# Kernel tuning notes

Measured on AMD Instinct MI355X. Metric: run time of the kernel, lower is better.

The kernel has to match this reference:

```python
import jax, jax.numpy as jnp
import numpy as np

N_NODES = 200000
N_EDGES = 3200000
DIM = 64


def setup_inputs() -> dict:
    key = jax.random.key(0)
    ks = jax.random.split(key, 8)
    ego = jax.random.normal(ks[0], (N_NODES, DIM), dtype=jnp.float32) * 0.1
    W1 = jax.random.normal(ks[1], (DIM, DIM), dtype=jnp.float32) * (1.0 / np.sqrt(DIM))
    b1 = jnp.zeros((DIM,), dtype=jnp.float32)
    W2 = jax.random.normal(ks[2], (DIM, DIM), dtype=jnp.float32) * (1.0 / np.sqrt(DIM))
    b2 = jnp.zeros((DIM,), dtype=jnp.float32)
    edge_row = jax.random.randint(ks[3], (N_EDGES,), 0, N_NODES, dtype=jnp.int32)
    edge_col = jax.random.randint(ks[4], (N_EDGES,), 0, N_NODES, dtype=jnp.int32)
    edge_val = jax.random.uniform(ks[5], (N_EDGES,), dtype=jnp.float32)
    return {"ego_embeddings": ego, "W1": W1, "b1": b1, "W2": W2, "b2": b2,
            "edge_row": edge_row, "edge_col": edge_col, "edge_val": edge_val}


def reference(ego_embeddings, W1, b1, W2, b2, edge_row, edge_col, edge_val):
    # side = A_in @ ego : sparse COO matmul via gather + weighted segment-sum
    gathered = ego_embeddings[edge_col] * edge_val[:, None]        # [E, D]
    side = jax.ops.segment_sum(gathered, edge_row, num_segments=N_NODES)  # [N, D]
    # bi-interaction aggregator (KGAT): LeakyReLU(negative_slope=0.01)
    sum_emb = jax.nn.leaky_relu((ego_embeddings + side) @ W1 + b1)
    bi_emb = jax.nn.leaky_relu((ego_embeddings * side) @ W2 + b2)
    return sum_emb + bi_emb  # dropout=0.0 -> identity
```

## Files before the change

kernel.cpp:

```cpp
#include <hip/hip_runtime.h>

#define DIM 64
#define SCAN_T 256
#define SCAN_E 8
#define SCAN_CHUNK (SCAN_T * SCAN_E)
#define BSHIFT 9
#define BROWS (1 << BSHIFT)
#define PBLK 512
#define MAXBUK 512

typedef unsigned int u32;
typedef unsigned long long u64;
typedef unsigned short u16;

__device__ __forceinline__ u32 packCV(int col, float v) {
    int q = (int)(v * 16384.f + 0.5f);
    q = min(q, 16383);
    return ((u32)col << 14) | (u32)q;
}

__device__ __forceinline__ u16 f2bf(float f) {
    u32 u = __float_as_uint(f);
    u32 r = u + 0x7FFFu + ((u >> 16) & 1u);
    return (u16)(r >> 16);
}
__device__ __forceinline__ float bf2f(u16 h) {
    return __uint_as_float((u32)h << 16);
}

__global__ void cvt_k(const float* __restrict__ src, u16* __restrict__ dst, int n4) {
    int i = blockIdx.x * blockDim.x + threadIdx.x;
    if (i < n4) {
        float4 f = reinterpret_cast<const float4*>(src)[i];
        ushort4 h;
        h.x = f2bf(f.x); h.y = f2bf(f.y); h.z = f2bf(f.z); h.w = f2bf(f.w);
        reinterpret_cast<ushort4*>(dst)[i] = h;
    }
}


__global__ __launch_bounds__(256) void histb_k(const int* __restrict__ erow,
                                               int* __restrict__ bhist,
                                               int E, int CH, int nbuk) {
    __shared__ int h[MAXBUK];
    const int tid = threadIdx.x;
    for (int i = tid; i < nbuk; i += 256) h[i] = 0;
    __syncthreads();
    const int s = blockIdx.x * CH;
    const int e = min(E, s + CH);
    for (int i4 = s + tid * 4; i4 < e; i4 += 256 * 4) {
        if (i4 + 3 < e) {
            const int4 r = *reinterpret_cast<const int4*>(erow + i4);
            atomicAdd(&h[r.x >> BSHIFT], 1);
            atomicAdd(&h[r.y >> BSHIFT], 1);
            atomicAdd(&h[r.z >> BSHIFT], 1);
            atomicAdd(&h[r.w >> BSHIFT], 1);
        } else {
            for (int i = i4; i < e; ++i) atomicAdd(&h[erow[i] >> BSHIFT], 1);
        }
    }
    __syncthreads();
    for (int i = tid; i < nbuk; i += 256) bhist[i * PBLK + blockIdx.x] = h[i];
}

__global__ void bbase_k(int* __restrict__ bhist, int* __restrict__ bktTot) {
    __shared__ int sh[SCAN_T];
    const int bk  = blockIdx.x;
    const int tid = threadIdx.x;
    const int v0 = bhist[bk * PBLK + 2 * tid];
    const int v1 = bhist[bk * PBLK + 2 * tid + 1];
    sh[tid] = v0 + v1;
    __syncthreads();
    for (int off = 1; off < SCAN_T; off <<= 1) {
        int t = (tid >= off) ? sh[tid - off] : 0;
        __syncthreads();
        sh[tid] += t;
        __syncthreads();
    }
    const int excl = (tid == 0) ? 0 : sh[tid - 1];
    bhist[bk * PBLK + 2 * tid]     = excl;
    bhist[bk * PBLK + 2 * tid + 1] = excl + v0;
    if (tid == SCAN_T - 1) bktTot[bk] = sh[SCAN_T - 1];
}

__global__ void scanBk_k(const int* __restrict__ tot, int* __restrict__ base, int nbuk) {
    __shared__ int sh[MAXBUK + 1];
    const int tid = threadIdx.x;
    for (int i = tid; i < nbuk; i += 512) sh[i] = tot[i];
    __syncthreads();
    if (tid == 0) {
        int s = 0;
        for (int i = 0; i < nbuk; ++i) { int t = sh[i]; sh[i] = s; s += t; }
        sh[nbuk] = s;
    }
    __syncthreads();
    for (int i = tid; i <= nbuk; i += 512) base[i] = sh[i];
}

__global__ __launch_bounds__(256) void part_k(const int* __restrict__ erow,
                                              const int* __restrict__ ecol,
                                              const float* __restrict__ ev,
                                              const int* __restrict__ bhist,
                                              const int* __restrict__ bktBase,
                                              u32* __restrict__ tcv,
                                              u16* __restrict__ trow,
                                              int E, int CH, int nbuk) {
    __shared__ int cur[MAXBUK];
    const int tid = threadIdx.x;
    for (int i = tid; i < nbuk; i += 256)
        cur[i] = bktBase[i] + bhist[i * PBLK + blockIdx.x];
    __syncthreads();
    const int s = blockIdx.x * CH;
    const int e = min(E, s + CH);
    const int lm = BROWS - 1;
    for (int i4 = s + tid * 4; i4 < e; i4 += 256 * 4) {
        if (i4 + 3 < e) {
            const int4   r = *reinterpret_cast<const int4*>(erow + i4);
            const int4   c = *reinterpret_cast<const int4*>(ecol + i4);
            const float4 v = *reinterpret_cast<const float4*>(ev + i4);
            int p;
            p = atomicAdd(&cur[r.x >> BSHIFT], 1); tcv[p] = packCV(c.x, v.x); trow[p] = (u16)(r.x & lm);
            p = atomicAdd(&cur[r.y >> BSHIFT], 1); tcv[p] = packCV(c.y, v.y); trow[p] = (u16)(r.y & lm);
            p = atomicAdd(&cur[r.z >> BSHIFT], 1); tcv[p] = packCV(c.z, v.z); trow[p] = (u16)(r.z & lm);
            p = atomicAdd(&cur[r.w >> BSHIFT], 1); tcv[p] = packCV(c.w, v.w); trow[p] = (u16)(r.w & lm);
        } else {
            for (int i = i4; i < e; ++i) {
                const int r = erow[i];
                const int p = atomicAdd(&cur[r >> BSHIFT], 1);
                tcv[p] = packCV(ecol[i], ev[i]);
                trow[p] = (u16)(r & lm);
            }
        }
    }
}

__global__ __launch_bounds__(512) void final2_k(const u32* __restrict__ tcv,
                                                const u16* __restrict__ trow,
                                                const int* __restrict__ bktBase,
                                                int* __restrict__ offs,
                                                u32* __restrict__ scv,
                                                int N, int nbuk) {
    __shared__ int rcur[BROWS];
    __shared__ int sc[BROWS];
    const int tid  = threadIdx.x;
    const int bk   = blockIdx.x;
    const int row0 = bk << BSHIFT;
    const int rows = min(BROWS, N - row0);
    const int s = bktBase[bk];
    const int e = bktBase[bk + 1];
    rcur[tid] = 0;
    __syncthreads();
    for (int i = s + tid; i < e; i += 512) atomicAdd(&rcur[trow[i]], 1);
    __syncthreads();
    sc[tid] = rcur[tid];
    __syncthreads();
    for (int off = 1; off < BROWS; off <<= 1) {
        int t = (tid >= off) ? sc[tid - off] : 0;
        __syncthreads();
        sc[tid] += t;
        __syncthreads();
    }
    const int excl = (tid == 0) ? 0 : sc[tid - 1];
    rcur[tid] = s + excl;
    if (tid < rows) offs[row0 + tid] = s + excl;
    if (bk == nbuk - 1 && tid == 0) offs[N] = e;
    __syncthreads();
    for (int i = s + tid; i < e; i += 512) {
        const u32 cv = tcv[i];
        const int lr = trow[i];
        const int p = atomicAdd(&rcur[lr], 1);
        scv[p] = cv;
    }
}

__global__ void hist_k(const int* __restrict__ erow, int* __restrict__ cnt, int E) {
    const int e4 = (blockIdx.x * blockDim.x + threadIdx.x) * 4;
    if (e4 + 3 < E) {
        const int4 r = *reinterpret_cast<const int4*>(erow + e4);
        atomicAdd(&cnt[r.x], 1);
        atomicAdd(&cnt[r.y], 1);
        atomicAdd(&cnt[r.z], 1);
        atomicAdd(&cnt[r.w], 1);
    } else {
        for (int e = e4; e < E; ++e) atomicAdd(&cnt[erow[e]], 1);
    }
}

__global__ void scanA_k(const int* __restrict__ cnt, int* __restrict__ offs,
                        int* __restrict__ bsums, int N) {
    __shared__ int sh[SCAN_T];
    const int base = blockIdx.x * SCAN_CHUNK + threadIdx.x * SCAN_E;
    int v[SCAN_E];
    int s = 0;
#pragma unroll
    for (int j = 0; j < SCAN_E; ++j) {
        int idx = base + j;
        int c = (idx < N) ? cnt[idx] : 0;
        v[j] = s;
        s += c;
    }
    sh[threadIdx.x] = s;
    __syncthreads();
    for (int off = 1; off < SCAN_T; off <<= 1) {
        int t = (threadIdx.x >= off) ? sh[threadIdx.x - off] : 0;
        __syncthreads();
        sh[threadIdx.x] += t;
        __syncthreads();
    }
    const int excl = (threadIdx.x == 0) ? 0 : sh[threadIdx.x - 1];
    if (threadIdx.x == SCAN_T - 1) bsums[blockIdx.x] = sh[SCAN_T - 1];
#pragma unroll
    for (int j = 0; j < SCAN_E; ++j) {
        int idx = base + j;
        if (idx < N) offs[idx] = v[j] + excl;
    }
}

__global__ void scanB_k(int* __restrict__ bsums, int nb) {
    __shared__ int sh[1024];
    const int tid = threadIdx.x;
    if (tid < nb) sh[tid] = bsums[tid];
    __syncthreads();
    if (tid == 0) {
        int s = 0;
        for (int i = 0; i < nb; ++i) { int t = sh[i]; sh[i] = s; s += t; }
    }
    __syncthreads();
    if (tid < nb) bsums[tid] = sh[tid];
}

__global__ void scanC_k(int* __restrict__ offs, int* __restrict__ cursor,
                        const int* __restrict__ bsums, int N, int E) {
    const int i = blockIdx.x * blockDim.x + threadIdx.x;
    if (i < N) {
        int v = offs[i] + bsums[i / SCAN_CHUNK];
        offs[i] = v;
        cursor[i] = v;
    }
    if (i == 0) offs[N] = E;
}

__global__ void reorder_k(const int* __restrict__ erow, const int* __restrict__ ecol,
                          const float* __restrict__ ev, int* __restrict__ cursor,
                          u32* __restrict__ scv, int E) {
    const int e4 = (blockIdx.x * blockDim.x + threadIdx.x) * 4;
    if (e4 + 3 < E) {
        const int4   r = *reinterpret_cast<const int4*>(erow + e4);
        const int4   c = *reinterpret_cast<const int4*>(ecol + e4);
        const float4 v = *reinterpret_cast<const float4*>(ev + e4);
        int p;
        p = atomicAdd(&cursor[r.x], 1); scv[p] = packCV(c.x, v.x);
        p = atomicAdd(&cursor[r.y], 1); scv[p] = packCV(c.y, v.y);
        p = atomicAdd(&cursor[r.z], 1); scv[p] = packCV(c.z, v.z);
        p = atomicAdd(&cursor[r.w], 1); scv[p] = packCV(c.w, v.w);
    } else {
        for (int e = e4; e < E; ++e) {
            int p = atomicAdd(&cursor[erow[e]], 1);
            scv[p] = packCV(ecol[e], ev[e]);
        }
    }
}

__device__ __forceinline__ float lrelu(float x) {
    return fmaxf(x, 0.f) + 0.01f * fminf(x, 0.f);
}

template <bool BF16>
__global__ __launch_bounds__(256, 2) void fused_k(const float* __restrict__ ego,
                                                  const u16* __restrict__ egoh,
                                                  const float* __restrict__ W1,
                                                  const float* __restrict__ b1,
                                                  const float* __restrict__ W2,
                                                  const float* __restrict__ b2,
                                                  const int* __restrict__ offs,
                                                  const u32* __restrict__ scv,
                                                  float* __restrict__ out,
                                                  int N, int rowsPerWave) {
    __shared__ __align__(16) float xsh[4][2][DIM];
    const int lane = threadIdx.x & 63;
    const int wid  = threadIdx.x >> 6;

    float w1[DIM], w2[DIM];
#pragma unroll
    for (int k = 0; k < DIM; ++k) {
        w1[k] = W1[k * DIM + lane];
        w2[k] = W2[k * DIM + lane];
    }
    const float bb1 = b1[lane];
    const float bb2 = b2[lane];

    const int waveId = blockIdx.x * 4 + wid;
    const int r0 = waveId * rowsPerWave;
    const int r1 = min(N, r0 + rowsPerWave);

    for (int row = r0; row < r1; ++row) {
        const int s = offs[row];
        const int t = offs[row + 1];
        float acc = 0.f;
        for (int base = s; base < t; base += 64) {
            const int m = min(64, t - base);
            const u32 cv = (lane < m) ? scv[base + lane] : 0u;
            for (int j = 0; j < m; j += 8) {
                u32 uu[8];
#pragma unroll
                for (int i = 0; i < 8; ++i) {
                    const int sj = j + i;
                    const u32 x = (u32)__shfl((int)cv, sj & 63);
                    uu[i] = (sj < m) ? x : 0u;
                }
                float g[8];
#pragma unroll
                for (int i = 0; i < 8; ++i) {
                    if (BF16) g[i] = bf2f(egoh[(uu[i] >> 14) * DIM + lane]);
                    else      g[i] = ego[(uu[i] >> 14) * DIM + lane];
                }
                const float sc = 1.f / 16384.f;
#pragma unroll
                for (int i = 0; i < 8; ++i)
                    acc = fmaf((float)(uu[i] & 16383u) * sc, g[i], acc);
            }
        }
        const int obase = row * DIM + lane;
        const float e = ego[obase];
        xsh[wid][0][lane] = e + acc;
        xsh[wid][1][lane] = e * acc;
        float a1 = bb1, a2 = bb2;
#pragma unroll
        for (int k4 = 0; k4 < 16; ++k4) {
            const float4 xa = *reinterpret_cast<const float4*>(&xsh[wid][0][k4 * 4]);
            const float4 xm = *reinterpret_cast<const float4*>(&xsh[wid][1][k4 * 4]);
            a1 = fmaf(xa.x, w1[4 * k4 + 0], a1);
            a1 = fmaf(xa.y, w1[4 * k4 + 1], a1);
            a1 = fmaf(xa.z, w1[4 * k4 + 2], a1);
            a1 = fmaf(xa.w, w1[4 * k4 + 3], a1);
            a2 = fmaf(xm.x, w2[4 * k4 + 0], a2);
            a2 = fmaf(xm.y, w2[4 * k4 + 1], a2);
            a2 = fmaf(xm.z, w2[4 * k4 + 2], a2);
            a2 = fmaf(xm.w, w2[4 * k4 + 3], a2);
        }
        out[obase] = lrelu(a1) + lrelu(a2);
    }
}

__device__ __forceinline__ void atomAddF(float* p, float v) {
    __hip_atomic_fetch_add(p, v, __ATOMIC_RELAXED, __HIP_MEMORY_SCOPE_AGENT);
}

__global__ void scatter_k(const float* __restrict__ ego,
                          const int* __restrict__ erow,
                          const int* __restrict__ ecol,
                          const float* __restrict__ eval_,
                          float* __restrict__ side,
                          long long total16) {
    long long tid = (long long)blockIdx.x * blockDim.x + threadIdx.x;
    if (tid >= total16) return;
    const int e = (int)(tid >> 4);
    const int q = (int)(tid & 15);
    const float4 g = *reinterpret_cast<const float4*>(ego + (size_t)ecol[e] * DIM + q * 4);
    const float v = eval_[e];
    float* dst = side + (size_t)erow[e] * DIM + q * 4;
    atomAddF(dst + 0, g.x * v);
    atomAddF(dst + 1, g.y * v);
    atomAddF(dst + 2, g.z * v);
    atomAddF(dst + 3, g.w * v);
}

__global__ __launch_bounds__(256) void mlp_k(const float* __restrict__ ego,
                                             const float* __restrict__ W1,
                                             const float* __restrict__ b1,
                                             const float* __restrict__ W2,
                                             const float* __restrict__ b2,
                                             float* out, int nNodes) {
    __shared__ __align__(16) float xsh[4][2][DIM];
    const int lane = threadIdx.x & 63;
    const int wid  = threadIdx.x >> 6;
    float w1[DIM], w2[DIM];
#pragma unroll
    for (int k = 0; k < DIM; ++k) {
        w1[k] = W1[k * DIM + lane];
        w2[k] = W2[k * DIM + lane];
    }
    const float bb1 = b1[lane];
    const float bb2 = b2[lane];
    const int waveId = blockIdx.x * 4 + wid;
    const int nWaves = gridDim.x * 4;
    for (int n = waveId; n < nNodes; n += nWaves) {
        const size_t base = (size_t)n * DIM + lane;
        const float e = ego[base];
        const float s = out[base];
        xsh[wid][0][lane] = e + s;
        xsh[wid][1][lane] = e * s;
        float acc1 = bb1, acc2 = bb2;
#pragma unroll
        for (int k4 = 0; k4 < 16; ++k4) {
            const float4 a = *reinterpret_cast<const float4*>(&xsh[wid][0][k4 * 4]);
            const float4 m = *reinterpret_cast<const float4*>(&xsh[wid][1][k4 * 4]);
            acc1 = fmaf(a.x, w1[4 * k4 + 0], acc1);
            acc1 = fmaf(a.y, w1[4 * k4 + 1], acc1);
            acc1 = fmaf(a.z, w1[4 * k4 + 2], acc1);
            acc1 = fmaf(a.w, w1[4 * k4 + 3], acc1);
            acc2 = fmaf(m.x, w2[4 * k4 + 0], acc2);
            acc2 = fmaf(m.y, w2[4 * k4 + 1], acc2);
            acc2 = fmaf(m.z, w2[4 * k4 + 2], acc2);
            acc2 = fmaf(m.w, w2[4 * k4 + 3], acc2);
        }
        const float r1 = fmaxf(acc1, 0.f) + 0.01f * fminf(acc1, 0.f);
        const float r2 = fmaxf(acc2, 0.f) + 0.01f * fminf(acc2, 0.f);
        out[base] = r1 + r2;
    }
}

extern "C" void kernel_launch(void* const* d_in, const int* in_sizes, int n_in,
                              void* d_out, int out_size, void* d_ws, size_t ws_size,
                              hipStream_t stream) {
    const float* ego  = (const float*)d_in[0];
    const float* W1   = (const float*)d_in[1];
    const float* b1   = (const float*)d_in[2];
    const float* W2   = (const float*)d_in[3];
    const float* b2   = (const float*)d_in[4];
    const int*   erow = (const int*)d_in[5];
    const int*   ecol = (const int*)d_in[6];
    const float* ev   = (const float*)d_in[7];
    float* out = (float*)d_out;

    const int N = in_sizes[0] / DIM;
    const int E = in_sizes[5];

    auto align256 = [](size_t x) { return (x + 63) & ~(size_t)63; };
    const int nbuk = (N + BROWS - 1) >> BSHIFT;

    size_t o_cnt     = 0;
    size_t o_offs    = align256(o_cnt + N);
    size_t o_cursor  = align256(o_offs + N + 1);
    size_t o_bsums   = align256(o_cursor + N);
    size_t o_scv     = align256(o_bsums + 1024);
    size_t o_egoh    = align256(o_scv + E);
    size_t o_bhist   = align256(o_egoh + (size_t)N * (DIM / 2));
    size_t o_bktTot  = align256(o_bhist + (size_t)MAXBUK * PBLK);
    size_t o_bktBase = align256(o_bktTot + MAXBUK);
    size_t o_tcv     = align256(o_bktBase + MAXBUK + 1);
    size_t o_trow    = align256(o_tcv + E);
    size_t need_main = (o_trow + (size_t)(E + 1) / 2) * sizeof(int);
    size_t need_fb1  = (o_bhist) * sizeof(int);
    size_t need_fb2  = (o_egoh) * sizeof(int);

    const bool packOK = (N <= (1 << 18));

    if (!packOK || ws_size < need_fb2) {
        hipMemsetAsync(out, 0, (size_t)out_size * sizeof(float), stream);
        const long long total16 = (long long)E * 16;
        scatter_k<<<(int)((total16 + 255) / 256), 256, 0, stream>>>(ego, erow, ecol, ev, out, total16);
        mlp_k<<<1024, 256, 0, stream>>>(ego, W1, b1, W2, b2, out, N);
        return;
    }

    int* ws = (int*)d_ws;
    int* cnt     = ws + o_cnt;
    int* offs    = ws + o_offs;
    int* cursor  = ws + o_cursor;
    int* bsums   = ws + o_bsums;
    u32* scv     = (u32*)(ws + o_scv);
    u16* egoh    = (u16*)(ws + o_egoh);
    int* bhist   = ws + o_bhist;
    int* bktTot  = ws + o_bktTot;
    int* bktBase = ws + o_bktBase;
    u32* tcv     = (u32*)(ws + o_tcv);
    u16* trow    = (u16*)(ws + o_trow);

    const bool useBF16  = ws_size >= need_fb1;
    const bool useRadix = (ws_size >= need_main) && (nbuk <= MAXBUK) && useBF16;

    if (useRadix) {
        const int CH = (((E + PBLK - 1) / PBLK) + 3) & ~3;
        histb_k<<<PBLK, 256, 0, stream>>>(erow, bhist, E, CH, nbuk);
        bbase_k<<<nbuk, SCAN_T, 0, stream>>>(bhist, bktTot);
        scanBk_k<<<1, 512, 0, stream>>>(bktTot, bktBase, nbuk);
        part_k<<<PBLK, 256, 0, stream>>>(erow, ecol, ev, bhist, bktBase, tcv, trow, E, CH, nbuk);
        final2_k<<<nbuk, 512, 0, stream>>>(tcv, trow, bktBase, offs, scv, N, nbuk);
        const int n4 = N * DIM / 4;
        cvt_k<<<(n4 + 255) / 256, 256, 0, stream>>>(ego, egoh, n4);
    } else {
        const int nb = (N + SCAN_CHUNK - 1) / SCAN_CHUNK;
        hipMemsetAsync(cnt, 0, (size_t)N * sizeof(int), stream);
        hist_k<<<(E / 4 + 255) / 256, 256, 0, stream>>>(erow, cnt, E);
        if (useBF16) {
            const int n4 = N * DIM / 4;
            cvt_k<<<(n4 + 255) / 256, 256, 0, stream>>>(ego, egoh, n4);
        }
        scanA_k<<<nb, SCAN_T, 0, stream>>>(cnt, offs, bsums, N);
        scanB_k<<<1, 1024, 0, stream>>>(bsums, nb);
        scanC_k<<<(N + 255) / 256, 256, 0, stream>>>(offs, cursor, bsums, N, E);
        reorder_k<<<(E / 4 + 255) / 256, 256, 0, stream>>>(erow, ecol, ev, cursor, scv, E);
    }

    const int nBlocks = 2048;
    const int nWaves = nBlocks * 4;
    const int rowsPerWave = (N + nWaves - 1) / nWaves;
    if (useBF16) {
        fused_k<true><<<nBlocks, 256, 0, stream>>>(ego, egoh, W1, b1, W2, b2, offs, scv, out, N, rowsPerWave);
    } else {
        fused_k<false><<<nBlocks, 256, 0, stream>>>(ego, egoh, W1, b1, W2, b2, offs, scv, out, N, rowsPerWave);
    }
}
```

Measured before the change: 313.5 us.

## Split wave into two half-waves gathering two edges with paired column loads

The gather loop now has each half of the wave handle a different edge. Each lane loads two adjacent columns per edge, as a 32-bit bf16 pair or a float2, so one wave instruction covers two edges with wider memory accesses. The halves are combined with a cross-lane xor shuffle, and the quantization scale is applied once at the end instead of per edge. The matvec epilogue switches to packed two-wide FMAs with weights stored as pairs. The trade-off is an extra reduction shuffle per row and half-wave lanes idling on rows with few edges.

```diff
diff --git a/kernel.cpp b/kernel.cpp
--- a/kernel.cpp
+++ b/kernel.cpp
@@ -12,6 +12,21 @@
 typedef unsigned int u32;
 typedef unsigned long long u64;
 typedef unsigned short u16;
+
+typedef float f32x2 __attribute__((ext_vector_type(2)));
+
+__device__ __forceinline__ f32x2 mk2(float a, float b) {
+    f32x2 r; r.x = a; r.y = b; return r;
+}
+
+#if __has_builtin(__builtin_elementwise_fma)
+#define FMA2(a, b, c) __builtin_elementwise_fma((a), (b), (c))
+#else
+__device__ __forceinline__ f32x2 fma2_(f32x2 a, f32x2 b, f32x2 c) {
+    f32x2 r; r.x = fmaf(a.x, b.x, c.x); r.y = fmaf(a.y, b.y, c.y); return r;
+}
+#define FMA2(a, b, c) fma2_((a), (b), (c))
+#endif
 
 __device__ __forceinline__ u32 packCV(int col, float v) {
     int q = (int)(v * 16384.f + 0.5f);
@@ -279,15 +294,20 @@
     __shared__ __align__(16) float xsh[4][2][DIM];
     const int lane = threadIdx.x & 63;
     const int wid  = threadIdx.x >> 6;
-
-    float w1[DIM], w2[DIM];
-#pragma unroll
-    for (int k = 0; k < DIM; ++k) {
-        w1[k] = W1[k * DIM + lane];
-        w2[k] = W2[k * DIM + lane];
+    const int q    = lane & 31;
+    const int half = lane >> 5;
+
+    f32x2 w1p[DIM / 2], w2p[DIM / 2];
+#pragma unroll
+    for (int k2 = 0; k2 < DIM / 2; ++k2) {
+        w1p[k2] = mk2(W1[(2 * k2) * DIM + lane], W1[(2 * k2 + 1) * DIM + lane]);
+        w2p[k2] = mk2(W2[(2 * k2) * DIM + lane], W2[(2 * k2 + 1) * DIM + lane]);
     }
     const float bb1 = b1[lane];
     const float bb2 = b2[lane];
+
+    const char* egob = (const char*)egoh + (size_t)q * 4;
+    const char* egof = (const char*)ego  + (size_t)q * 8;
 
     const int waveId = blockIdx.x * 4 + wid;
     const int r0 = waveId * rowsPerWave;
@@ -296,49 +316,61 @@
     for (int row = r0; row < r1; ++row) {
         const int s = offs[row];
         const int t = offs[row + 1];
-        float acc = 0.f;
+        f32x2 acc = mk2(0.f, 0.f);
         for (int base = s; base < t; base += 64) {
             const int m = min(64, t - base);
             const u32 cv = (lane < m) ? scv[base + lane] : 0u;
-            for (int j = 0; j < m; j += 8) {
+            for (int j0 = 0; j0 < m; j0 += 16) {
                 u32 uu[8];
 #pragma unroll
                 for (int i = 0; i < 8; ++i) {
-                    const int sj = j + i;
-                    const u32 x = (u32)__shfl((int)cv, sj & 63);
-                    uu[i] = (sj < m) ? x : 0u;
+                    const int e = j0 + 2 * i + half;
+                    const u32 x = (u32)__shfl((int)cv, e & 63);
+                    uu[i] = (e < m) ? x : 0u;
                 }
-                float g[8];
+                f32x2 g[8];
 #pragma unroll
                 for (int i = 0; i < 8; ++i) {
-                    if (BF16) g[i] = bf2f(egoh[(uu[i] >> 14) * DIM + lane]);
-                    else      g[i] = ego[(uu[i] >> 14) * DIM + lane];
+                    const u32 col = uu[i] >> 14;
+                    if (BF16) {
+                        const u32 gb = *reinterpret_cast<const u32*>(egob + ((size_t)col << 7));
+                        g[i] = mk2(__uint_as_float(gb << 16),
+                                   __uint_as_float(gb & 0xFFFF0000u));
+                    } else {
+                        g[i] = *reinterpret_cast<const f32x2*>(egof + ((size_t)col << 8));
+                    }
                 }
-                const float sc = 1.f / 16384.f;
-#pragma unroll
-                for (int i = 0; i < 8; ++i)
-                    acc = fmaf((float)(uu[i] & 16383u) * sc, g[i], acc);
+#pragma unroll
+                for (int i = 0; i < 8; ++i) {
+                    const float val = (float)(uu[i] & 16383u);
+                    acc = FMA2(mk2(val, val), g[i], acc);
+                }
             }
         }
-        const int obase = row * DIM + lane;
-        const float e = ego[obase];
-        xsh[wid][0][lane] = e + acc;
-        xsh[wid][1][lane] = e * acc;
-        float a1 = bb1, a2 = bb2;
-#pragma unroll
-        for (int k4 = 0; k4 < 16; ++k4) {
-            const float4 xa = *reinterpret_cast<const float4*>(&xsh[wid][0][k4 * 4]);
-            const float4 xm = *reinterpret_cast<const float4*>(&xsh[wid][1][k4 * 4]);
-            a1 = fmaf(xa.x, w1[4 * k4 + 0], a1);
-            a1 = fmaf(xa.y, w1[4 * k4 + 1], a1);
-            a1 = fmaf(xa.z, w1[4 * k4 + 2], a1);
-            a1 = fmaf(xa.w, w1[4 * k4 + 3], a1);
-            a2 = fmaf(xm.x, w2[4 * k4 + 0], a2);
-            a2 = fmaf(xm.y, w2[4 * k4 + 1], a2);
-            a2 = fmaf(xm.z, w2[4 * k4 + 2], a2);
-            a2 = fmaf(xm.w, w2[4 * k4 + 3], a2);
-        }
-        out[obase] = lrelu(a1) + lrelu(a2);
+        acc.x += __shfl_xor(acc.x, 32);
+        acc.y += __shfl_xor(acc.y, 32);
+        const float sc = 1.f / 16384.f;
+        const f32x2 sd = mk2(acc.x * sc, acc.y * sc);
+        const f32x2 e2 = *reinterpret_cast<const f32x2*>(ego + (size_t)row * DIM + 2 * q);
+        const f32x2 x1 = e2 + sd;
+        const f32x2 x2 = e2 * sd;
+        if (half == 0) {
+            *reinterpret_cast<f32x2*>(&xsh[wid][0][2 * q]) = x1;
+            *reinterpret_cast<f32x2*>(&xsh[wid][1][2 * q]) = x2;
+        }
+        f32x2 a1p = mk2(0.f, 0.f), a2p = mk2(0.f, 0.f);
+#pragma unroll
+        for (int k4 = 0; k4 < DIM / 4; ++k4) {
+            const float4 xa = *reinterpret_cast<const float4*>(&xsh[wid][0][4 * k4]);
+            const float4 xm = *reinterpret_cast<const float4*>(&xsh[wid][1][4 * k4]);
+            a1p = FMA2(mk2(xa.x, xa.y), w1p[2 * k4],     a1p);
+            a1p = FMA2(mk2(xa.z, xa.w), w1p[2 * k4 + 1], a1p);
+            a2p = FMA2(mk2(xm.x, xm.y), w2p[2 * k4],     a2p);
+            a2p = FMA2(mk2(xm.z, xm.w), w2p[2 * k4 + 1], a2p);
+        }
+        const float a1 = a1p.x + a1p.y + bb1;
+        const float a2 = a2p.x + a2p.y + bb2;
+        out[(size_t)row * DIM + lane] = lrelu(a1) + lrelu(a2);
     }
 }
 
@@ -355,10 +387,10 @@
     long long tid = (long long)blockIdx.x * blockDim.x + threadIdx.x;
     if (tid >= total16) return;
     const int e = (int)(tid >> 4);
-    const int q = (int)(tid & 15);
-    const float4 g = *reinterpret_cast<const float4*>(ego + (size_t)ecol[e] * DIM + q * 4);
+    const int qq = (int)(tid & 15);
+    const float4 g = *reinterpret_cast<const float4*>(ego + (size_t)ecol[e] * DIM + qq * 4);
     const float v = eval_[e];
-    float* dst = side + (size_t)erow[e] * DIM + q * 4;
+    float* dst = side + (size_t)erow[e] * DIM + qq * 4;
     atomAddF(dst + 0, g.x * v);
     atomAddF(dst + 1, g.y * v);
     atomAddF(dst + 2, g.z * v);
```

New measurement: 346.9 us. +10.6%, slower.
